# Optimization experiments

Hardware: AMD Instinct MI355X
Metric: run time of the kernel (lower is better)

Reference implementation:

```python
import jax, jax.numpy as jnp
import numpy as np

NUM_HEADS, NUM_KV, HEAD_DIM, WIDTH = 4, 1, 256, 1024
MASK_FILL = -2.3819763e38


def _apply_rope(x, positions, max_wavelength=10000.0):
    # x: [B, T, N, H], positions: [B, T]
    d = x.shape[-1]
    freq_exp = (2.0 / d) * jnp.arange(d // 2, dtype=jnp.float32)
    timescale = max_wavelength ** freq_exp                      # [H/2]
    radians = positions[..., None].astype(jnp.float32) / timescale  # [B, T, H/2]
    radians = radians[..., None, :]                             # [B, T, 1, H/2]
    sin, cos = jnp.sin(radians), jnp.cos(radians)
    x1, x2 = jnp.split(x, 2, axis=-1)
    out = jnp.concatenate([x1 * cos - x2 * sin, x2 * cos + x1 * sin], axis=-1)
    return out.astype(x.dtype)


def _rmsnorm(x, scale):
    var = jnp.mean(jnp.square(x.astype(jnp.float32)), axis=-1, keepdims=True)
    normed = x * jax.lax.rsqrt(var + 1e-6)
    return (normed * (1 + scale)).astype(x.dtype)


def setup_inputs() -> dict:
    key = jax.random.key(0)
    ks = jax.random.split(key, 7)
    B, T, S = 8, 512, 2048
    return {
        "x": jax.random.normal(ks[0], (B, T, WIDTH), jnp.float32),
        "mem_seq": jax.random.normal(ks[1], (B, S, WIDTH), jnp.float32),
        "mem_mask": jax.random.randint(ks[2], (B, S), 0, 2).astype(bool),
        "rms_scale": jax.random.normal(ks[3], (WIDTH,), jnp.float32) * 0.02,
        "q_w": jax.random.normal(ks[4], (NUM_HEADS, WIDTH, HEAD_DIM), jnp.float32) / np.sqrt(WIDTH),
        "kv_w": jax.random.normal(ks[5], (2, NUM_KV, WIDTH, HEAD_DIM), jnp.float32) / np.sqrt(WIDTH),
        "out_w": jax.random.normal(ks[6], (NUM_HEADS, HEAD_DIM, WIDTH), jnp.float32) / np.sqrt(NUM_HEADS * HEAD_DIM),
    }


def reference(x, mem_seq, mem_mask, rms_scale, q_w, kv_w, out_w):
    B, S, _ = mem_seq.shape
    T = x.shape[1]
    G = NUM_HEADS // NUM_KV  # query heads per kv head

    xn = _rmsnorm(x, rms_scale)          # shared RMSNorm params
    mn = _rmsnorm(mem_seq, rms_scale)

    q = jnp.einsum("BTD,NDH->BTNH", xn, q_w)          # [B,T,4,256]
    kv = jnp.einsum("BSD,cKDH->cBSKH", mn, kv_w)      # [2,B,S,1,256]
    k, v = kv[0], kv[1]

    q_pos = jnp.broadcast_to(jnp.arange(S, T + S), (B, T))
    k_pos = jnp.broadcast_to(jnp.arange(S), (B, S))
    q = _apply_rope(q, q_pos) * (HEAD_DIM ** -0.5)
    k = _apply_rope(k, k_pos)

    q = q.reshape(B, T, NUM_KV, G, HEAD_DIM)
    logits = jnp.einsum("BTKGH,BSKH->BKGTS", q, k, preferred_element_type=jnp.float32)
    masked = jnp.where(mem_mask[:, None, None, None, :], logits, MASK_FILL)
    probs = jax.nn.softmax(masked, axis=-1).astype(x.dtype)
    enc = jnp.einsum("BKGTS,BSKH->BTKGH", probs, v).reshape(B, T, NUM_HEADS, HEAD_DIM)
    return jnp.einsum("BTNH,NHD->BTD", enc, out_w)
```

## Files before the change

kernel.cpp:

```cpp
#include <hip/hip_runtime.h>
#include <stdint.h>

typedef __bf16   bf16x8 __attribute__((ext_vector_type(8)));
typedef float    f32x4  __attribute__((ext_vector_type(4)));
typedef float    f32x16 __attribute__((ext_vector_type(16)));
typedef uint16_t u16x8  __attribute__((ext_vector_type(8)));
typedef uint16_t u16x4  __attribute__((ext_vector_type(4)));
typedef uint32_t u32x4  __attribute__((ext_vector_type(4)));

#define DEVFN static __device__ __forceinline__

DEVFN uint16_t f2bf(float f){
  uint32_t u = __builtin_bit_cast(uint32_t, f);
  u += 0x7fffu + ((u >> 16) & 1u);
  return (uint16_t)(u >> 16);
}
DEVFN float bf2f(uint16_t h){
  return __builtin_bit_cast(float, (uint32_t)h << 16);
}
DEVFN bf16x8 ldbf8(const uint16_t* p){
  return __builtin_bit_cast(bf16x8, *(const u16x8*)p);
}
DEVFN void gl16(const void* g, void* l){
  __builtin_amdgcn_global_load_lds((__attribute__((address_space(1))) void*)g,
                                   (__attribute__((address_space(3))) void*)l,
                                   16, 0, 0);
}
DEVFN f32x4 mfma16(bf16x8 a, bf16x8 b, f32x4 c){
  return __builtin_amdgcn_mfma_f32_16x16x32_bf16(a, b, c, 0, 0, 0);
}
DEVFN f32x16 mfma32(bf16x8 a, bf16x8 b, f32x16 c){
  return __builtin_amdgcn_mfma_f32_32x32x16_bf16(a, b, c, 0, 0, 0);
}
DEVFN uint32_t cvtpk(float lo, float hi){
  uint32_t r;
  asm("v_cvt_pk_bf16_f32 %0, %1, %2" : "=v"(r) : "v"(lo), "v"(hi));
  return r;
}
DEVFN void plswap(uint32_t &x, uint32_t &y){
  asm("v_permlane32_swap_b32 %0, %1" : "+v"(x), "+v"(y));
}

__global__ void detect_mask_k(const uint32_t* m, int* flag){
  int i = blockIdx.x * 256 + threadIdx.x;
  uint32_t v = m[i];
  int notint   = (v > 1u) ? 1 : 0;
  int notfloat = (v != 0u && v != 0x3F800000u) ? 2 : 0;
  int bits = notint | notfloat;
  if (__any(bits)){
    int agg = bits;
    agg |= __shfl_xor(agg, 1);  agg |= __shfl_xor(agg, 2);
    agg |= __shfl_xor(agg, 4);  agg |= __shfl_xor(agg, 8);
    agg |= __shfl_xor(agg, 16); agg |= __shfl_xor(agg, 32);
    if ((threadIdx.x & 63) == 0) atomicOr(flag, agg);
  }
}

__global__ void expand_mask_k(const void* m, const int* flag, float* bias){
  int i = blockIdx.x * 256 + threadIdx.x;
  int f = *flag;
  bool on;
  if ((f & 1) == 0)      on = ((const int*)m)[i]   != 0;
  else if ((f & 2) == 0) on = ((const float*)m)[i] != 0.0f;
  else                   on = ((const uint8_t*)m)[i] != 0;
  bias[i] = on ? 0.0f : -1e30f;
}

__global__ __launch_bounds__(256) void rmsnorm_k(const float* __restrict__ x,
                                                 const float* __restrict__ mem,
                                                 uint16_t* __restrict__ xn,
                                                 uint16_t* __restrict__ mn,
                                                 const float* __restrict__ scale){
  int row = blockIdx.x;
  const float* in; uint16_t* out; int r0;
  if (row < 4096){ in = x;  out = xn; r0 = row; }
  else           { in = mem; out = mn; r0 = row - 4096; }
  const float4* ip = (const float4*)(in + (size_t)r0 * 1024);
  float4 v = ip[threadIdx.x];
  float ss = v.x*v.x + v.y*v.y + v.z*v.z + v.w*v.w;
  #pragma unroll
  for (int off = 1; off < 64; off <<= 1) ss += __shfl_xor(ss, off);
  __shared__ float wsum[4];
  if ((threadIdx.x & 63) == 0) wsum[threadIdx.x >> 6] = ss;
  __syncthreads();
  float r = rsqrtf((wsum[0] + wsum[1] + wsum[2] + wsum[3]) * (1.0f/1024.0f) + 1e-6f);
  float4 sc = ((const float4*)scale)[threadIdx.x];
  u16x4 o;
  o[0] = f2bf(v.x * r * (1.0f + sc.x));
  o[1] = f2bf(v.y * r * (1.0f + sc.y));
  o[2] = f2bf(v.z * r * (1.0f + sc.z));
  o[3] = f2bf(v.w * r * (1.0f + sc.w));
  *(u16x4*)(out + (size_t)r0 * 1024 + threadIdx.x * 4) = o;
}

__global__ void transpose_cast_all_k(const float* __restrict__ qw,
                                     const float* __restrict__ kvw,
                                     const float* __restrict__ ow,
                                     uint16_t* __restrict__ wq,
                                     uint16_t* __restrict__ wkv,
                                     uint16_t* __restrict__ wout){
  int z = blockIdx.z;
  const float* in; uint16_t* out; int rs, os, C;
  if (z < 4)      { in = qw  + z*262144;     out = wq  + z*262144;     rs = 256;  os = 1024; C = 256; }
  else if (z < 6) { in = kvw + (z-4)*262144; out = wkv + (z-4)*262144; rs = 256;  os = 1024; C = 256; }
  else            { in = ow;                 out = wout;               rs = 1024; os = 1024; C = 1024; }
  int c0 = blockIdx.x * 32, r0 = blockIdx.y * 32;
  if (c0 >= C) return;
  __shared__ float t[32][33];
  int tx = threadIdx.x, ty = threadIdx.y;
  #pragma unroll
  for (int i = 0; i < 4; ++i)
    t[ty + 8*i][tx] = in[(size_t)(r0 + ty + 8*i) * rs + c0 + tx];
  __syncthreads();
  #pragma unroll
  for (int i = 0; i < 4; ++i)
    out[(size_t)(c0 + ty + 8*i) * os + r0 + tx] = f2bf(t[tx][ty + 8*i]);
}

__global__ __launch_bounds__(256) void rope_all_k(uint16_t* q, uint16_t* kk){
  if (blockIdx.x < 8192){
    int idx = blockIdx.x * 256 + threadIdx.x;
    int j = idx & 127, n = (idx >> 7) & 3, bt = idx >> 9;
    float inv = exp2f((float)j * (-13.287712379549449f / 128.0f));
    float rad = (float)(2048 + (bt & 511)) * inv;
    float s, c; sincosf(rad, &s, &c);
    size_t base = (size_t)bt * 1024 + n * 256 + j;
    float x1 = bf2f(q[base]), x2 = bf2f(q[base + 128]);
    q[base]       = f2bf((x1 * c - x2 * s) * 0.0625f);
    q[base + 128] = f2bf((x2 * c + x1 * s) * 0.0625f);
  } else {
    int idx = (blockIdx.x - 8192) * 256 + threadIdx.x;
    int j = idx & 127, bs = idx >> 7;
    float inv = exp2f((float)j * (-13.287712379549449f / 128.0f));
    float rad = (float)(bs & 2047) * inv;
    float s, c; sincosf(rad, &s, &c);
    size_t base = (size_t)bs * 256 + j;
    float x1 = bf2f(kk[base]), x2 = bf2f(kk[base + 128]);
    kk[base]       = f2bf(x1 * c - x2 * s);
    kk[base + 128] = f2bf(x2 * c + x1 * s);
  }
}

#define GEMM_BODY(A_, Bt_, K_)                                                  \
  __shared__ __align__(16) uint16_t As[128*64];                                 \
  __shared__ __align__(16) uint16_t Bs[128*64];                                 \
  f32x4 acc[4][4] = {};                                                         \
  {                                                                             \
    const int K = (K_);                                                         \
    _Pragma("unroll 1")                                                         \
    for (int k0 = 0; k0 < K; k0 += 64){                                         \
      __syncthreads();                                                          \
      _Pragma("unroll")                                                         \
      for (int it = 0; it < 4; ++it){                                           \
        int ob = it * 4096 + tid * 16;                                          \
        int row = ob >> 7;                                                      \
        int col = (ob & 127) ^ ((row & 7) << 4);                                \
        gl16((const char*)(A_)  + ((size_t)(m0 + row) * K + k0) * 2 + col,      \
             (char*)As + it * 4096 + wid * 1024);                               \
        gl16((const char*)(Bt_) + ((size_t)(n0 + row) * K + k0) * 2 + col,      \
             (char*)Bs + it * 4096 + wid * 1024);                               \
      }                                                                         \
      __syncthreads();                                                          \
      bf16x8 af[2][4], bfr[2][4];                                               \
      _Pragma("unroll")                                                         \
      for (int ks = 0; ks < 2; ++ks){                                           \
        _Pragma("unroll")                                                       \
        for (int m = 0; m < 4; ++m)                                             \
          af[ks][m]  = ldbf8(&As[(wr*64 + m*16 + lr) * 64 +                     \
                                 ((ks*32 + lq*8) ^ ((lr & 7) << 3))]);          \
        _Pragma("unroll")                                                       \
        for (int n = 0; n < 4; ++n)                                             \
          bfr[ks][n] = ldbf8(&Bs[(wc*64 + n*16 + lr) * 64 +                     \
                                 ((ks*32 + lq*8) ^ ((lr & 7) << 3))]);          \
      }                                                                         \
      _Pragma("unroll")                                                         \
      for (int ks = 0; ks < 2; ++ks)                                            \
        _Pragma("unroll")                                                       \
        for (int m = 0; m < 4; ++m)                                             \
          _Pragma("unroll")                                                     \
          for (int n = 0; n < 4; ++n)                                           \
            acc[m][n] = mfma16(af[ks][m], bfr[ks][n], acc[m][n]);               \
    }                                                                           \
  }

__global__ __launch_bounds__(256) void gemm_qkv_k(const uint16_t* __restrict__ xn,
                                                  const uint16_t* __restrict__ mn,
                                                  const uint16_t* __restrict__ wq,
                                                  const uint16_t* __restrict__ wkv,
                                                  uint16_t* __restrict__ qb,
                                                  uint16_t* __restrict__ kb,
                                                  uint16_t* __restrict__ vt3){
  int bx = blockIdx.x;
  bool isq = bx < 256;
  const uint16_t *A, *Bt;
  int n0, m0;
  if (isq){ A = xn; Bt = wq;  n0 = (bx & 7) * 128;  m0 = (bx >> 3) * 128; }
  else    { int b2 = bx - 256; A = mn; Bt = wkv; n0 = (b2 & 3) * 128; m0 = (b2 >> 2) * 128; }
  int tid = threadIdx.x, lane = tid & 63, wid = tid >> 6;
  int wr = wid >> 1, wc = wid & 1;
  int lr = lane & 15, lq = lane >> 4;
  GEMM_BODY(A, Bt, 1024)
  #pragma unroll
  for (int m = 0; m < 4; ++m)
    #pragma unroll
    for (int n = 0; n < 4; ++n){
      int gr0 = m0 + wr*64 + m*16 + lq*4;
      int gc  = n0 + wc*64 + n*16 + lr;
      if (isq){
        #pragma unroll
        for (int r = 0; r < 4; ++r) qb[(size_t)(gr0 + r) * 1024 + gc] = f2bf(acc[m][n][r]);
      } else if (gc < 256){
        #pragma unroll
        for (int r = 0; r < 4; ++r) kb[(size_t)(gr0 + r) * 256 + gc] = f2bf(acc[m][n][r]);
      } else {
        int h = gc - 256, bb = gr0 >> 11, s0 = gr0 & 2047;
        int st = s0 >> 5, sc = (s0 >> 3) & 3, s8 = s0 & 7;
        u16x4 pk;
        #pragma unroll
        for (int r = 0; r < 4; ++r) pk[r] = f2bf(acc[m][n][r]);
        *(u16x4*)&vt3[((((size_t)bb*64 + st)*4 + sc)*256 + h)*8 + s8] = pk;
      }
    }
}

__global__ __launch_bounds__(256) void gemm_out_k(const uint16_t* __restrict__ A,
                                                  const uint16_t* __restrict__ Bt,
                                                  float* __restrict__ Cf){
  int n0 = blockIdx.x * 128, m0 = blockIdx.y * 128;
  int tid = threadIdx.x, lane = tid & 63, wid = tid >> 6;
  int wr = wid >> 1, wc = wid & 1;
  int lr = lane & 15, lq = lane >> 4;
  GEMM_BODY(A, Bt, 1024)
  #pragma unroll
  for (int m = 0; m < 4; ++m)
    #pragma unroll
    for (int n = 0; n < 4; ++n){
      int gr0 = m0 + wr*64 + m*16 + lq*4;
      int gc  = n0 + wc*64 + n*16 + lr;
      #pragma unroll
      for (int r = 0; r < 4; ++r) Cf[(size_t)(gr0 + r) * 1024 + gc] = acc[m][n][r];
    }
}

__global__ __launch_bounds__(512, 2) void attn_k(const uint16_t* __restrict__ Q,
                                                 const uint16_t* __restrict__ Kb,
                                                 const uint16_t* __restrict__ Vt3,
                                                 const float* __restrict__ bias,
                                                 uint16_t* __restrict__ po,
                                                 uint16_t* __restrict__ po3,
                                                 float* __restrict__ pm,
                                                 float* __restrict__ pl){
  int bx = blockIdx.x;
  int b = bx & 7, qt = (bx >> 3) & 7, sh = bx >> 6;
  int tid = threadIdx.x, lane = tid & 63, wid = tid >> 6;
  int n = wid & 3, qs = wid >> 2;
  int lc = lane & 31, hi = lane >> 5;
  __shared__ __align__(16) uint16_t Ks[3*32*256];
  __shared__ __align__(16) uint16_t Vs[3*4*256*8];
  __shared__ uint32_t mask_lds[16];

  int sbeg = sh * 512;
  {
    float bv = bias[b*2048 + sbeg + tid];
    unsigned long long bal = __ballot(bv == 0.0f);
    if (lane == 0){
      mask_lds[wid*2]     = (uint32_t)bal;
      mask_lds[wid*2 + 1] = (uint32_t)(bal >> 32);
    }
  }

  int t0w = qt*64 + qs*32;
  bf16x8 qf[16];
  {
    const uint16_t* qp = Q + (size_t)(b*512 + t0w + lc) * 1024 + n*256 + hi*8;
    #pragma unroll
    for (int kc = 0; kc < 16; ++kc) qf[kc] = ldbf8(qp + kc*16);
  }
  f32x16 o[8] = {};
  float mrow = -1e30f, lrow = 0.0f;

  auto STAGE = [&](int buf, int s0){
    const char* vsrc = (const char*)Vt3 + ((size_t)(b*64 + (s0 >> 5))) * 16384;
    #pragma unroll
    for (int it = 0; it < 2; ++it){
      int ob = it*8192 + tid*16;
      int krow = ob >> 9;
      int kcol = (ob & 511) ^ ((krow & 7) << 4);
      gl16((const char*)Kb + ((size_t)(b*2048 + s0 + krow) * 256) * 2 + kcol,
           (char*)Ks + buf*16384 + it*8192 + wid*1024);
      gl16(vsrc + ob,
           (char*)Vs + buf*16384 + it*8192 + wid*1024);
    }
  };

  STAGE(0, sbeg);
  STAGE(1, sbeg + 32);

  #pragma unroll 1
  for (int t = 0; t < 16; ++t){
    if (t == 0)      asm volatile("s_waitcnt vmcnt(4) lgkmcnt(0)" ::: "memory");
    else if (t < 15) asm volatile("s_waitcnt vmcnt(4)" ::: "memory");
    else             asm volatile("s_waitcnt vmcnt(0)" ::: "memory");
    __builtin_amdgcn_s_barrier();
    asm volatile("" ::: "memory");
    if (t < 14) STAGE((t+2)%3, sbeg + (t+2)*32);

    const uint16_t* ksb = Ks + (t%3)*8192;
    const uint16_t* vsb = Vs + (t%3)*8192;

    f32x16 sacc = {};
    __builtin_amdgcn_s_setprio(1);
    #pragma unroll
    for (int kc = 0; kc < 16; ++kc){
      bf16x8 ak = ldbf8(&ksb[lc*256 + ((kc*16 + hi*8) ^ ((lc & 7) << 3))]);
      sacc = mfma32(ak, qf[kc], sacc);
    }
    __builtin_amdgcn_s_setprio(0);

    uint32_t mw = mask_lds[t];
    int sb4 = hi * 4;
    float p[16];
    float mx = -1e30f;
    #pragma unroll
    for (int r = 0; r < 16; ++r){
      int sr = (r & 3) + 8*(r >> 2) + sb4;
      float v = ((mw >> sr) & 1u) ? sacc[r] : -1e30f;
      p[r] = v;
      mx = fmaxf(mx, v);
    }
    mx = fmaxf(mx, __shfl_xor(mx, 32));
    if (__any(mx > mrow + 8.0f)){
      float mn = fmaxf(mrow, mx);
      float scl = __expf(mrow - mn);
      mrow = mn; lrow *= scl;
      #pragma unroll
      for (int ht = 0; ht < 8; ++ht) o[ht] *= scl;
    }
    float rs = 0.0f;
    #pragma unroll
    for (int r = 0; r < 16; ++r){ p[r] = __expf(p[r] - mrow); rs += p[r]; }
    rs += __shfl_xor(rs, 32);
    lrow += rs;

    uint32_t w0, w1, w2, w3, w4, w5, w6, w7;
    w0 = cvtpk(p[0], p[1]);   w2 = cvtpk(p[4], p[5]);   plswap(w0, w2);
    w1 = cvtpk(p[2], p[3]);   w3 = cvtpk(p[6], p[7]);   plswap(w1, w3);
    w4 = cvtpk(p[8], p[9]);   w6 = cvtpk(p[12], p[13]); plswap(w4, w6);
    w5 = cvtpk(p[10], p[11]); w7 = cvtpk(p[14], p[15]); plswap(w5, w7);
    u32x4 t0v = {w0, w1, w2, w3};
    u32x4 t1v = {w4, w5, w6, w7};
    bf16x8 pa0 = __builtin_bit_cast(bf16x8, t0v);
    bf16x8 pa1 = __builtin_bit_cast(bf16x8, t1v);

    __builtin_amdgcn_s_setprio(1);
    #pragma unroll
    for (int ht = 0; ht < 8; ++ht){
      bf16x8 bv0 = ldbf8(&vsb[(size_t)hi*2048       + (ht*32 + lc)*8]);
      o[ht] = mfma32(pa0, bv0, o[ht]);
      bf16x8 bv1 = ldbf8(&vsb[(size_t)(2 + hi)*2048 + (ht*32 + lc)*8]);
      o[ht] = mfma32(pa1, bv1, o[ht]);
    }
    __builtin_amdgcn_s_setprio(0);
  }

  uint16_t* pop = (sh == 3) ? po3 : po + (size_t)sh * 4194304;
  #pragma unroll
  for (int ht = 0; ht < 8; ++ht)
    #pragma unroll
    for (int r = 0; r < 16; ++r){
      int qr = (r & 3) + 8*(r >> 2) + hi*4;
      pop[(size_t)(b*512 + t0w + qr)*1024 + n*256 + ht*32 + lc] = f2bf(o[ht][r]);
    }
  if (hi == 0){
    int mlidx = sh*16384 + (b*512 + t0w + lc)*4 + n;
    pm[mlidx] = mrow;
    pl[mlidx] = lrow;
  }
}

__global__ __launch_bounds__(64) void merge_k(const uint16_t* __restrict__ po,
                                              const uint16_t* __restrict__ po3,
                                              const float* __restrict__ pm,
                                              const float* __restrict__ pl,
                                              uint16_t* __restrict__ enc){
  int idx = blockIdx.x;
  int row = idx >> 2, n = idx & 3;
  float m = -1e30f;
  #pragma unroll
  for (int h = 0; h < 4; ++h) m = fmaxf(m, pm[h*16384 + idx]);
  float w[4], lsum = 0.0f;
  #pragma unroll
  for (int h = 0; h < 4; ++h){
    w[h] = __expf(pm[h*16384 + idx] - m);
    lsum += pl[h*16384 + idx] * w[h];
  }
  float inv = 1.0f / lsum;
  size_t off = (size_t)row*1024 + n*256 + threadIdx.x*4;
  float acc[4] = {0.f, 0.f, 0.f, 0.f};
  #pragma unroll
  for (int h = 0; h < 4; ++h){
    const uint16_t* src = (h < 3) ? po + (size_t)h*4194304 + off : po3 + off;
    u16x4 a = *(const u16x4*)src;
    #pragma unroll
    for (int r = 0; r < 4; ++r) acc[r] += bf2f(a[r]) * w[h];
  }
  u16x4 ov;
  #pragma unroll
  for (int r = 0; r < 4; ++r) ov[r] = f2bf(acc[r] * inv);
  *(u16x4*)(enc + off) = ov;
}

extern "C" void kernel_launch(void* const* d_in, const int* in_sizes, int n_in,
                              void* d_out, int out_size, void* d_ws, size_t ws_size,
                              hipStream_t stream){
  const float* x    = (const float*)d_in[0];
  const float* mem  = (const float*)d_in[1];
  const void*  mask = d_in[2];
  const float* rms  = (const float*)d_in[3];
  const float* qw   = (const float*)d_in[4];
  const float* kvw  = (const float*)d_in[5];
  const float* ow   = (const float*)d_in[6];
  float* out = (float*)d_out;
  char* ws = (char*)d_ws;

  uint16_t* xn   = (uint16_t*)(ws + 0);
  uint16_t* enc  = (uint16_t*)(ws + 0);
  const size_t MB = 1ull << 20;
  uint16_t* qb   = (uint16_t*)(ws + 8*MB);
  uint16_t* kb   = (uint16_t*)(ws + 16*MB);
  uint16_t* vt3  = (uint16_t*)(ws + 24*MB);
  uint16_t* wq   = (uint16_t*)(ws + 32*MB);
  float*    pm   = (float*)   (ws + 32*MB);
  float*    pl   = (float*)   (ws + 32*MB + 262144);
  uint16_t* wkv  = (uint16_t*)(ws + 34*MB);
  uint16_t* wout = (uint16_t*)(ws + 35*MB);
  float*    bias = (float*)   (ws + 37*MB);
  int*      flag = (int*)     (ws + 37*MB + 65536);
  uint16_t* mn   = (uint16_t*)(ws + 38*MB);
  uint16_t* po   = (uint16_t*)(ws + 38*MB);
  uint16_t* po3  = (uint16_t*)out;

  hipMemsetAsync(flag, 0, 4, stream);
  detect_mask_k<<<16, 256, 0, stream>>>((const uint32_t*)mask, flag);
  expand_mask_k<<<64, 256, 0, stream>>>(mask, flag, bias);

  rmsnorm_k<<<20480, 256, 0, stream>>>(x, mem, xn, mn, rms);

  transpose_cast_all_k<<<dim3(32,32,7), dim3(32,8), 0, stream>>>(qw, kvw, ow, wq, wkv, wout);

  gemm_qkv_k<<<768, 256, 0, stream>>>(xn, mn, wq, wkv, qb, kb, vt3);

  rope_all_k<<<16384, 256, 0, stream>>>(qb, kb);

  attn_k<<<256, 512, 0, stream>>>(qb, kb, vt3, bias, po, po3, pm, pl);
  merge_k<<<16384, 64, 0, stream>>>(po, po3, pm, pl, enc);

  gemm_out_k<<<dim3(8, 32), 256, 0, stream>>>(enc, wout, out);
}
```

Baseline: 173.3 us.

## Fuse RoPE into QKV GEMM epilogue and attention, merge pre-kernels

```diff
diff --git a/kernel.cpp b/kernel.cpp
--- a/kernel.cpp
+++ b/kernel.cpp
@@ -39,6 +39,9 @@
 }
 DEVFN void plswap(uint32_t &x, uint32_t &y){
   asm("v_permlane32_swap_b32 %0, %1" : "+v"(x), "+v"(y));
+}
+DEVFN int permcol(int j){
+  return (((j & 127) >> 4) << 5) + (((j >> 7) & 1) << 4) + (j & 15);
 }
 
 __global__ void detect_mask_k(const uint32_t* m, int* flag){
@@ -66,78 +69,61 @@
   bias[i] = on ? 0.0f : -1e30f;
 }
 
-__global__ __launch_bounds__(256) void rmsnorm_k(const float* __restrict__ x,
-                                                 const float* __restrict__ mem,
-                                                 uint16_t* __restrict__ xn,
-                                                 uint16_t* __restrict__ mn,
-                                                 const float* __restrict__ scale){
-  int row = blockIdx.x;
-  const float* in; uint16_t* out; int r0;
-  if (row < 4096){ in = x;  out = xn; r0 = row; }
-  else           { in = mem; out = mn; r0 = row - 4096; }
-  const float4* ip = (const float4*)(in + (size_t)r0 * 1024);
-  float4 v = ip[threadIdx.x];
-  float ss = v.x*v.x + v.y*v.y + v.z*v.z + v.w*v.w;
-  #pragma unroll
-  for (int off = 1; off < 64; off <<= 1) ss += __shfl_xor(ss, off);
-  __shared__ float wsum[4];
-  if ((threadIdx.x & 63) == 0) wsum[threadIdx.x >> 6] = ss;
-  __syncthreads();
-  float r = rsqrtf((wsum[0] + wsum[1] + wsum[2] + wsum[3]) * (1.0f/1024.0f) + 1e-6f);
-  float4 sc = ((const float4*)scale)[threadIdx.x];
-  u16x4 o;
-  o[0] = f2bf(v.x * r * (1.0f + sc.x));
-  o[1] = f2bf(v.y * r * (1.0f + sc.y));
-  o[2] = f2bf(v.z * r * (1.0f + sc.z));
-  o[3] = f2bf(v.w * r * (1.0f + sc.w));
-  *(u16x4*)(out + (size_t)r0 * 1024 + threadIdx.x * 4) = o;
-}
-
-__global__ void transpose_cast_all_k(const float* __restrict__ qw,
-                                     const float* __restrict__ kvw,
-                                     const float* __restrict__ ow,
-                                     uint16_t* __restrict__ wq,
-                                     uint16_t* __restrict__ wkv,
-                                     uint16_t* __restrict__ wout){
-  int z = blockIdx.z;
-  const float* in; uint16_t* out; int rs, os, C;
-  if (z < 4)      { in = qw  + z*262144;     out = wq  + z*262144;     rs = 256;  os = 1024; C = 256; }
-  else if (z < 6) { in = kvw + (z-4)*262144; out = wkv + (z-4)*262144; rs = 256;  os = 1024; C = 256; }
-  else            { in = ow;                 out = wout;               rs = 1024; os = 1024; C = 1024; }
-  int c0 = blockIdx.x * 32, r0 = blockIdx.y * 32;
-  if (c0 >= C) return;
-  __shared__ float t[32][33];
-  int tx = threadIdx.x, ty = threadIdx.y;
-  #pragma unroll
-  for (int i = 0; i < 4; ++i)
-    t[ty + 8*i][tx] = in[(size_t)(r0 + ty + 8*i) * rs + c0 + tx];
-  __syncthreads();
-  #pragma unroll
-  for (int i = 0; i < 4; ++i)
-    out[(size_t)(c0 + ty + 8*i) * os + r0 + tx] = f2bf(t[tx][ty + 8*i]);
-}
-
-__global__ __launch_bounds__(256) void rope_all_k(uint16_t* q, uint16_t* kk){
-  if (blockIdx.x < 8192){
-    int idx = blockIdx.x * 256 + threadIdx.x;
-    int j = idx & 127, n = (idx >> 7) & 3, bt = idx >> 9;
-    float inv = exp2f((float)j * (-13.287712379549449f / 128.0f));
-    float rad = (float)(2048 + (bt & 511)) * inv;
-    float s, c; sincosf(rad, &s, &c);
-    size_t base = (size_t)bt * 1024 + n * 256 + j;
-    float x1 = bf2f(q[base]), x2 = bf2f(q[base + 128]);
-    q[base]       = f2bf((x1 * c - x2 * s) * 0.0625f);
-    q[base + 128] = f2bf((x2 * c + x1 * s) * 0.0625f);
+__global__ __launch_bounds__(256) void fused_pre_k(const float* __restrict__ x,
+                                                   const float* __restrict__ mem,
+                                                   uint16_t* __restrict__ xn,
+                                                   uint16_t* __restrict__ mn,
+                                                   const float* __restrict__ scale,
+                                                   const float* __restrict__ qw,
+                                                   const float* __restrict__ kvw,
+                                                   const float* __restrict__ ow,
+                                                   uint16_t* __restrict__ wq,
+                                                   uint16_t* __restrict__ wkv,
+                                                   uint16_t* __restrict__ wout){
+  int bid = blockIdx.x;
+  if (bid < 20480){
+    int row = bid;
+    const float* in; uint16_t* out; int r0;
+    if (row < 4096){ in = x;  out = xn; r0 = row; }
+    else           { in = mem; out = mn; r0 = row - 4096; }
+    const float4* ip = (const float4*)(in + (size_t)r0 * 1024);
+    float4 v = ip[threadIdx.x];
+    float ss = v.x*v.x + v.y*v.y + v.z*v.z + v.w*v.w;
+    #pragma unroll
+    for (int off = 1; off < 64; off <<= 1) ss += __shfl_xor(ss, off);
+    __shared__ float wsum[4];
+    if ((threadIdx.x & 63) == 0) wsum[threadIdx.x >> 6] = ss;
+    __syncthreads();
+    float r = rsqrtf((wsum[0] + wsum[1] + wsum[2] + wsum[3]) * (1.0f/1024.0f) + 1e-6f);
+    float4 sc = ((const float4*)scale)[threadIdx.x];
+    u16x4 o;
+    o[0] = f2bf(v.x * r * (1.0f + sc.x));
+    o[1] = f2bf(v.y * r * (1.0f + sc.y));
+    o[2] = f2bf(v.z * r * (1.0f + sc.z));
+    o[3] = f2bf(v.w * r * (1.0f + sc.w));
+    *(u16x4*)(out + (size_t)r0 * 1024 + threadIdx.x * 4) = o;
   } else {
-    int idx = (blockIdx.x - 8192) * 256 + threadIdx.x;
-    int j = idx & 127, bs = idx >> 7;
-    float inv = exp2f((float)j * (-13.287712379549449f / 128.0f));
-    float rad = (float)(bs & 2047) * inv;
-    float s, c; sincosf(rad, &s, &c);
-    size_t base = (size_t)bs * 256 + j;
-    float x1 = bf2f(kk[base]), x2 = bf2f(kk[base + 128]);
-    kk[base]       = f2bf(x1 * c - x2 * s);
-    kk[base + 128] = f2bf(x2 * c + x1 * s);
+    int t = bid - 20480;
+    int z = t >> 10, rem = t & 1023;
+    int r0 = (rem >> 5) * 32, c0 = (rem & 31) * 32;
+    const float* in; uint16_t* out; int rs, C;
+    bool perm;
+    if (z < 4)      { in = qw  + z*262144;     out = wq  + z*262144;     rs = 256;  C = 256;  perm = true;  }
+    else if (z < 6) { in = kvw + (z-4)*262144; out = wkv + (z-4)*262144; rs = 256;  C = 256;  perm = (z == 4); }
+    else            { in = ow;                 out = wout;               rs = 1024; C = 1024; perm = false; }
+    if (c0 >= C) return;
+    __shared__ float tt[32][33];
+    int tx = threadIdx.x & 31, ty = threadIdx.x >> 5;
+    #pragma unroll
+    for (int i = 0; i < 4; ++i)
+      tt[ty + 8*i][tx] = in[(size_t)(r0 + ty + 8*i) * rs + c0 + tx];
+    __syncthreads();
+    #pragma unroll
+    for (int i = 0; i < 4; ++i){
+      int c = c0 + ty + 8*i;
+      int pc = perm ? permcol(c) : c;
+      out[(size_t)pc * 1024 + r0 + tx] = f2bf(tt[tx][ty + 8*i]);
+    }
   }
 }
 
@@ -200,19 +186,43 @@
   int wr = wid >> 1, wc = wid & 1;
   int lr = lane & 15, lq = lane >> 4;
   GEMM_BODY(A, Bt, 1024)
-  #pragma unroll
-  for (int m = 0; m < 4; ++m)
-    #pragma unroll
-    for (int n = 0; n < 4; ++n){
-      int gr0 = m0 + wr*64 + m*16 + lq*4;
-      int gc  = n0 + wc*64 + n*16 + lr;
-      if (isq){
+  if (isq){
+    #pragma unroll
+    for (int m = 0; m < 4; ++m)
+      #pragma unroll
+      for (int n = 0; n < 4; ++n){
+        int gr0 = m0 + wr*64 + m*16 + lq*4;
+        int gc  = n0 + wc*64 + n*16 + lr;
         #pragma unroll
         for (int r = 0; r < 4; ++r) qb[(size_t)(gr0 + r) * 1024 + gc] = f2bf(acc[m][n][r]);
-      } else if (gc < 256){
+      }
+  } else if (n0 < 256){
+    #pragma unroll
+    for (int m = 0; m < 4; ++m){
+      int gr0 = m0 + wr*64 + m*16 + lq*4;
+      #pragma unroll
+      for (int np = 0; np < 2; ++np){
+        int gcl = n0 + wc*64 + (2*np)*16 + lr;
+        int j = ((gcl >> 5) << 4) + (gcl & 15);
+        float inv = exp2f((float)j * (-13.287712379549449f / 128.0f));
         #pragma unroll
-        for (int r = 0; r < 4; ++r) kb[(size_t)(gr0 + r) * 256 + gc] = f2bf(acc[m][n][r]);
-      } else {
+        for (int r = 0; r < 4; ++r){
+          int s = (gr0 + r) & 2047;
+          float rad = (float)s * inv;
+          float sn, cs; sincosf(rad, &sn, &cs);
+          float x1 = acc[m][2*np][r], x2 = acc[m][2*np + 1][r];
+          kb[(size_t)(gr0 + r) * 256 + gcl]      = f2bf(x1*cs - x2*sn);
+          kb[(size_t)(gr0 + r) * 256 + gcl + 16] = f2bf(x2*cs + x1*sn);
+        }
+      }
+    }
+  } else {
+    #pragma unroll
+    for (int m = 0; m < 4; ++m)
+      #pragma unroll
+      for (int n = 0; n < 4; ++n){
+        int gr0 = m0 + wr*64 + m*16 + lq*4;
+        int gc  = n0 + wc*64 + n*16 + lr;
         int h = gc - 256, bb = gr0 >> 11, s0 = gr0 & 2047;
         int st = s0 >> 5, sc = (s0 >> 3) & 3, s8 = s0 & 7;
         u16x4 pk;
@@ -220,7 +230,7 @@
         for (int r = 0; r < 4; ++r) pk[r] = f2bf(acc[m][n][r]);
         *(u16x4*)&vt3[((((size_t)bb*64 + st)*4 + sc)*256 + h)*8 + s8] = pk;
       }
-    }
+  }
 }
 
 __global__ __launch_bounds__(256) void gemm_out_k(const uint16_t* __restrict__ A,
@@ -276,8 +286,6 @@
     #pragma unroll
     for (int kc = 0; kc < 16; ++kc) qf[kc] = ldbf8(qp + kc*16);
   }
-  f32x16 o[8] = {};
-  float mrow = -1e30f, lrow = 0.0f;
 
   auto STAGE = [&](int buf, int s0){
     const char* vsrc = (const char*)Vt3 + ((size_t)(b*64 + (s0 >> 5))) * 16384;
@@ -295,6 +303,31 @@
 
   STAGE(0, sbeg);
   STAGE(1, sbeg + 32);
+
+  {
+    float pos = (float)(2048 + t0w + lc);
+    #pragma unroll
+    for (int kp = 0; kp < 8; ++kp){
+      u16x8 a  = __builtin_bit_cast(u16x8, qf[2*kp]);
+      u16x8 bq = __builtin_bit_cast(u16x8, qf[2*kp + 1]);
+      u16x8 ra, rb;
+      #pragma unroll
+      for (int e = 0; e < 8; ++e){
+        int j = kp*16 + hi*8 + e;
+        float inv = exp2f((float)j * (-13.287712379549449f / 128.0f));
+        float rad = pos * inv;
+        float sn, cs; sincosf(rad, &sn, &cs);
+        float x1 = bf2f(a[e]), x2 = bf2f(bq[e]);
+        ra[e] = f2bf((x1*cs - x2*sn) * 0.0625f);
+        rb[e] = f2bf((x2*cs + x1*sn) * 0.0625f);
+      }
+      qf[2*kp]     = __builtin_bit_cast(bf16x8, ra);
+      qf[2*kp + 1] = __builtin_bit_cast(bf16x8, rb);
+    }
+  }
+
+  f32x16 o[8] = {};
+  float mrow = -1e30f, lrow = 0.0f;
 
   #pragma unroll 1
   for (int t = 0; t < 16; ++t){
@@ -444,13 +477,9 @@
   detect_mask_k<<<16, 256, 0, stream>>>((const uint32_t*)mask, flag);
   expand_mask_k<<<64, 256, 0, stream>>>(mask, flag, bias);
 
-  rmsnorm_k<<<20480, 256, 0, stream>>>(x, mem, xn, mn, rms);
-
-  transpose_cast_all_k<<<dim3(32,32,7), dim3(32,8), 0, stream>>>(qw, kvw, ow, wq, wkv, wout);
+  fused_pre_k<<<27648, 256, 0, stream>>>(x, mem, xn, mn, rms, qw, kvw, ow, wq, wkv, wout);
 
   gemm_qkv_k<<<768, 256, 0, stream>>>(xn, mn, wq, wkv, qb, kb, vt3);
-
-  rope_all_k<<<16384, 256, 0, stream>>>(qb, kb);
 
   attn_k<<<256, 512, 0, stream>>>(qb, kb, vt3, bias, po, po3, pm, pl);
   merge_k<<<16384, 64, 0, stream>>>(po, po3, pm, pl, enc);
```

After: 184.9 us. +6.7%, slower.
